# Kernel tuning notes

Hardware: AMD Instinct MI355X
Metric: run time of the kernel (lower is better)

Reference implementation:

```python
import jax, jax.numpy as jnp
import numpy as np

B, D, H = 8192, 1024, 1024


def _linear_init(key, shape, fan_in):
    bound = 1.0 / np.sqrt(fan_in)
    return jax.random.uniform(key, shape, jnp.float32, -bound, bound)


def setup_inputs() -> dict:
    key = jax.random.key(0)
    ks = jax.random.split(key, 20)
    inp = {
        "x": jax.random.normal(ks[0], (B, D), jnp.float32),
        "h_prev": jax.random.normal(ks[1], (B, H), jnp.float32),
        "c_prev": jax.random.normal(ks[2], (B, H), jnp.float32),
        "C_prev": jax.random.normal(ks[3], (B, H), jnp.float32),
        "n_prev": jax.random.uniform(ks[4], (B, H), jnp.float32),
        "m_prev": jax.random.normal(ks[5], (B, H), jnp.float32),
    }
    # input projections Wz/Wi/Wf/Wo: Linear(D -> H) with bias
    for i, g in enumerate("ziofo"[:4]):
        pass
    names = ["z", "i", "f", "o"]
    for j, g in enumerate(names):
        inp[f"W{g}"] = _linear_init(ks[6 + j], (H, D), D)
        inp[f"b{g}"] = _linear_init(ks[10 + j], (H,), D)
        inp[f"R{g}"] = _linear_init(ks[14 + j], (H, H), H)  # no bias
    return inp


def reference(x, h_prev, c_prev, C_prev, n_prev, m_prev,
              Wz, bz, Wi, bi, Wf, bf, Wo, bo,
              Rz, Ri, Rf, Ro):
    # Batch the 4 input projections and 4 recurrent projections into 2 GEMMs.
    Wcat = jnp.concatenate([Wi, Wf, Wo, Wz], axis=0)        # [4H, D]
    bcat = jnp.concatenate([bi, bf, bo, bz], axis=0)        # [4H]
    Rcat = jnp.concatenate([Ri, Rf, Ro, Rz], axis=0)        # [4H, H]
    pre = x @ Wcat.T + bcat + h_prev @ Rcat.T               # [B, 4H]
    pi, pf, po, pz = jnp.split(pre, 4, axis=1)

    i = jnp.exp(pi)
    f = jax.nn.sigmoid(pf)
    o = jax.nn.sigmoid(po)
    z = jnp.tanh(pz)

    c = f * c_prev + i * z
    n = f * n_prev + i
    m = jnp.maximum(jnp.log(f) + m_prev, pi)  # log(exp(pi)) == pi
    h = o * (c / n)
    return (h, c, C_prev, n, m)
```

## Files before the change

### kernel.cpp

```cpp
#include <hip/hip_runtime.h>


#define B_SZ 8192
#define D_SZ 1024
#define H_SZ 1024
#define K_SZ 2048
#define N4H  4096

typedef __attribute__((ext_vector_type(4))) float f32x4;
typedef _Float16 f16;
typedef __attribute__((ext_vector_type(8))) f16 f16x8;
typedef unsigned short u16;
typedef __attribute__((ext_vector_type(4))) unsigned short u16x4;

static __device__ __forceinline__ u16 f2h(float f) {
    f16 h = (f16)f;
    return __builtin_bit_cast(unsigned short, h);
}

static __device__ __forceinline__ float rcp_fast(float x) {
    float r;
    asm("v_rcp_f32 %0, %1" : "=v"(r) : "v"(x));
    return r;
}

static __device__ __forceinline__ void load_lds16(const void* g, void* l) {
    __builtin_amdgcn_global_load_lds(
        (const __attribute__((address_space(1))) void*)g,
        (__attribute__((address_space(3))) void*)l, 16, 0, 0);
}

__global__ void convert_AW(const float* __restrict__ x, const float* __restrict__ h,
                           const float* __restrict__ Wi, const float* __restrict__ Wf,
                           const float* __restrict__ Wo, const float* __restrict__ Wz,
                           const float* __restrict__ Ri, const float* __restrict__ Rf,
                           const float* __restrict__ Ro, const float* __restrict__ Rz,
                           const float* __restrict__ C_prev,
                           u16* __restrict__ A, u16* __restrict__ Wb,
                           float* __restrict__ outC) {
    const size_t nvecA = (size_t)B_SZ * K_SZ / 4;
    const size_t nvecW = (size_t)N4H * K_SZ / 4;
    const size_t nvecC = (size_t)B_SZ * H_SZ / 4;
    const size_t nvec  = nvecA + nvecW + nvecC;
    const size_t stride = (size_t)gridDim.x * blockDim.x;
    for (size_t v = (size_t)blockIdx.x * blockDim.x + threadIdx.x; v < nvec; v += stride) {
        if (v >= nvecA + nvecW) {
            size_t e = (v - nvecA - nvecW) * 4;
            *(f32x4*)&outC[e] = *(const f32x4*)&C_prev[e];
            continue;
        }
        const float* src;
        u16* dst;
        if (v < nvecA) {
            size_t e = v * 4;
            size_t row = e >> 11;
            int col = (int)(e & 2047);
            src = (col < D_SZ) ? (x + row * D_SZ + col)
                               : (h + row * H_SZ + (col - D_SZ));
            dst = A + e;
        } else {
            size_t e = (v - nvecA) * 4;
            size_t r = e >> 11;
            int col = (int)(e & 2047);
            int g = (int)(r >> 4) & 3;
            int j = (int)((r >> 6) << 4) | (int)(r & 15);
            const float* Wg = (g == 0) ? Wi : (g == 1) ? Wf : (g == 2) ? Wo : Wz;
            const float* Rg = (g == 0) ? Ri : (g == 1) ? Rf : (g == 2) ? Ro : Rz;
            src = (col < D_SZ) ? (Wg + (size_t)j * D_SZ + col)
                               : (Rg + (size_t)j * H_SZ + (col - D_SZ));
            dst = Wb + e;
        }
        f32x4 val = *(const f32x4*)src;
        u16x4 o;
        o[0] = f2h(val[0]); o[1] = f2h(val[1]); o[2] = f2h(val[2]); o[3] = f2h(val[3]);
        *(u16x4*)dst = o;
    }
}

__global__ __launch_bounds__(256, 2)
void gemm_fused(const u16* __restrict__ A, const u16* __restrict__ W,
                const float* __restrict__ c_prev, const float* __restrict__ n_prev,
                const float* __restrict__ m_prev,
                const float* __restrict__ bi, const float* __restrict__ bfv,
                const float* __restrict__ bo, const float* __restrict__ bz,
                float* __restrict__ out) {
    __shared__ char smem[49152];
    u16* lA = (u16*)smem;
    u16* lB = (u16*)(smem + 16384);
    float* eC = (float*)smem;
    float* eN = (float*)(smem + 16384);
    float* eM = (float*)(smem + 32768);

    const int tid = threadIdx.x;
    const int w  = tid >> 6;
    const int l  = tid & 63;
    const int wm = w >> 1;
    const int wn = w & 1;
    const int m0 = blockIdx.x * 128;
    const int n0 = blockIdx.y * 128;

    const int lrow8 = l >> 3;
    const int lseg  = (l & 7) ^ lrow8;

    const int fr = l & 15;
    const int kq = l >> 4;

    f32x4 acc[4][4] = {};

    for (int kt = 0; kt < K_SZ; kt += 64) {
#pragma unroll
        for (int r = 0; r < 4; ++r) {
            int rowA = r * 32 + w * 8 + lrow8;
            const u16* gA = A + (size_t)(m0 + rowA) * K_SZ + kt + lseg * 8;
            load_lds16(gA, (char*)lA + (r * 32 + w * 8) * 128);
            const u16* gB = W + (size_t)(n0 + rowA) * K_SZ + kt + lseg * 8;
            load_lds16(gB, (char*)lB + (r * 32 + w * 8) * 128);
        }
        __syncthreads();

#pragma unroll
        for (int ks = 0; ks < 2; ++ks) {
            f16x8 af[4], bfr[4];
#pragma unroll
            for (int mi = 0; mi < 4; ++mi) {
                int row = wm * 64 + mi * 16 + fr;
                int seg = (ks * 4 + kq) ^ (row & 7);
                af[mi] = *(const f16x8*)&lA[row * 64 + seg * 8];
            }
#pragma unroll
            for (int ni = 0; ni < 4; ++ni) {
                int row = wn * 64 + ni * 16 + fr;
                int seg = (ks * 4 + kq) ^ (row & 7);
                bfr[ni] = *(const f16x8*)&lB[row * 64 + seg * 8];
            }
#pragma unroll
            for (int mi = 0; mi < 4; ++mi)
#pragma unroll
                for (int ni = 0; ni < 4; ++ni)
                    acc[mi][ni] = __builtin_amdgcn_mfma_f32_16x16x32_f16(
                        af[mi], bfr[ni], acc[mi][ni], 0, 0, 0);
        }
        __syncthreads();
    }

    const int jbase = ((n0 + wn * 64) >> 6) * 16;
    {
        const size_t goff = (size_t)(m0 + wm * 64) * H_SZ + jbase;
        const float* cb = c_prev + goff;
        const float* nb = n_prev + goff;
        const float* mb = m_prev + goff;
        const size_t lsrc = (size_t)(l >> 2) * H_SZ + (l & 3) * 4;
#pragma unroll
        for (int k = 0; k < 4; ++k) {
            char* ldst_c = (char*)eC + w * 4096 + k * 1024;
            char* ldst_n = (char*)eN + w * 4096 + k * 1024;
            char* ldst_m = (char*)eM + w * 4096 + k * 1024;
            load_lds16(cb + (size_t)k * 16 * H_SZ + lsrc, ldst_c);
            load_lds16(nb + (size_t)k * 16 * H_SZ + lsrc, ldst_n);
            load_lds16(mb + (size_t)k * 16 * H_SZ + lsrc, ldst_m);
        }
    }

    const size_t BH = (size_t)B_SZ * H_SZ;
    const int j = jbase + fr;
    const float bvi = bi[j], bvf = bfv[j], bvo = bo[j], bvz = bz[j];

    asm volatile("s_waitcnt vmcnt(0)" ::: "memory");
    const int ebase = w * 1024;

#pragma unroll
    for (int mi = 0; mi < 4; ++mi) {
        const int rbase = m0 + wm * 64 + mi * 16 + kq * 4;
        const int erow0 = mi * 16 + kq * 4;
#pragma unroll
        for (int r2 = 0; r2 < 4; ++r2) {
            const size_t idx = (size_t)(rbase + r2) * H_SZ + j;
            const int eidx = ebase + (erow0 + r2) * 16 + fr;
            float pi = acc[mi][0][r2] + bvi;
            float pf = acc[mi][1][r2] + bvf;
            float po = acc[mi][2][r2] + bvo;
            float pz = acc[mi][3][r2] + bvz;
            float iv = __expf(pi);
            float fv = rcp_fast(1.0f + __expf(-pf));
            float ov = rcp_fast(1.0f + __expf(-po));
            float zv = 1.0f - 2.0f * rcp_fast(__expf(2.0f * pz) + 1.0f);
            float cv = fv * eC[eidx] + iv * zv;
            float nv = fv * eN[eidx] + iv;
            float mv = fmaxf(__logf(fv) + eM[eidx], pi);
            out[idx]          = ov * cv * rcp_fast(nv);
            out[BH + idx]     = cv;
            out[3 * BH + idx] = nv;
            out[4 * BH + idx] = mv;
        }
    }
}

extern "C" void kernel_launch(void* const* d_in, const int* in_sizes, int n_in,
                              void* d_out, int out_size, void* d_ws, size_t ws_size,
                              hipStream_t stream) {
    const float* x      = (const float*)d_in[0];
    const float* h_prev = (const float*)d_in[1];
    const float* c_prev = (const float*)d_in[2];
    const float* C_prev = (const float*)d_in[3];
    const float* n_prev = (const float*)d_in[4];
    const float* m_prev = (const float*)d_in[5];
    const float* Wz = (const float*)d_in[6];
    const float* bz = (const float*)d_in[7];
    const float* Rz = (const float*)d_in[8];
    const float* Wi = (const float*)d_in[9];
    const float* bi = (const float*)d_in[10];
    const float* Ri = (const float*)d_in[11];
    const float* Wf = (const float*)d_in[12];
    const float* bf = (const float*)d_in[13];
    const float* Rf = (const float*)d_in[14];
    const float* Wo = (const float*)d_in[15];
    const float* bo = (const float*)d_in[16];
    const float* Ro = (const float*)d_in[17];
    float* out = (float*)d_out;

    const size_t BH = (size_t)B_SZ * H_SZ;

    u16* Abuf = (u16*)d_ws;
    u16* Wbuf = (u16*)((char*)d_ws + (size_t)32 * 1024 * 1024);

    convert_AW<<<2048, 256, 0, stream>>>(x, h_prev, Wi, Wf, Wo, Wz,
                                         Ri, Rf, Ro, Rz, C_prev,
                                         Abuf, Wbuf, out + 2 * BH);

    gemm_fused<<<dim3(B_SZ / 128, N4H / 128), 256, 0, stream>>>(
        Abuf, Wbuf, c_prev, n_prev, m_prev, bi, bf, bo, bz, out);
}
```

Before: 210.4 us.

## Enlarge GEMM block tile to 256x128 with 512 threads and split epilogue

Doubles the M tile per block to 256 rows using 8 waves, so each block loads the W tile once for twice as many rows and global traffic for B drops. LDS is repartitioned into a 32KB A region and a 16KB B region. The epilogue now stages c/n/m_prev in two halves so the per-wave staging fits the reused LDS. Launch bounds of (512,4) put heavy pressure on the register budget and risk spills, while the grid halves in size, which could hurt load balance.

```diff
diff --git a/kernel.cpp b/kernel.cpp
--- a/kernel.cpp
+++ b/kernel.cpp
@@ -77,7 +77,7 @@
     }
 }
 
-__global__ __launch_bounds__(256, 2)
+__global__ __launch_bounds__(512, 4)
 void gemm_fused(const u16* __restrict__ A, const u16* __restrict__ W,
                 const float* __restrict__ c_prev, const float* __restrict__ n_prev,
                 const float* __restrict__ m_prev,
@@ -86,17 +86,14 @@
                 float* __restrict__ out) {
     __shared__ char smem[49152];
     u16* lA = (u16*)smem;
-    u16* lB = (u16*)(smem + 16384);
-    float* eC = (float*)smem;
-    float* eN = (float*)(smem + 16384);
-    float* eM = (float*)(smem + 32768);
+    u16* lB = (u16*)(smem + 32768);
 
     const int tid = threadIdx.x;
     const int w  = tid >> 6;
     const int l  = tid & 63;
     const int wm = w >> 1;
     const int wn = w & 1;
-    const int m0 = blockIdx.x * 128;
+    const int m0 = blockIdx.x * 256;
     const int n0 = blockIdx.y * 128;
 
     const int lrow8 = l >> 3;
@@ -107,17 +104,22 @@
 
     f32x4 acc[4][4] = {};
 
-    for (int kt = 0; kt < K_SZ; kt += 64) {
+    auto stage = [&](int kt) {
 #pragma unroll
         for (int r = 0; r < 4; ++r) {
-            int rowA = r * 32 + w * 8 + lrow8;
-            const u16* gA = A + (size_t)(m0 + rowA) * K_SZ + kt + lseg * 8;
-            load_lds16(gA, (char*)lA + (r * 32 + w * 8) * 128);
-            const u16* gB = W + (size_t)(n0 + rowA) * K_SZ + kt + lseg * 8;
-            load_lds16(gB, (char*)lB + (r * 32 + w * 8) * 128);
-        }
-        __syncthreads();
-
+            int row = r * 64 + w * 8 + lrow8;
+            const u16* gA = A + (size_t)(m0 + row) * K_SZ + kt + lseg * 8;
+            load_lds16(gA, (char*)lA + (r * 64 + w * 8) * 128);
+        }
+#pragma unroll
+        for (int r = 0; r < 2; ++r) {
+            int row = r * 64 + w * 8 + lrow8;
+            const u16* gB = W + (size_t)(n0 + row) * K_SZ + kt + lseg * 8;
+            load_lds16(gB, (char*)lB + (r * 64 + w * 8) * 128);
+        }
+    };
+
+    auto compute = [&]() {
 #pragma unroll
         for (int ks = 0; ks < 2; ++ks) {
             f16x8 af[4], bfr[4];
@@ -140,42 +142,47 @@
                     acc[mi][ni] = __builtin_amdgcn_mfma_f32_16x16x32_f16(
                         af[mi], bfr[ni], acc[mi][ni], 0, 0, 0);
         }
+    };
+
+    for (int kt = 0; kt < K_SZ; kt += 64) {
+        stage(kt);
+        __syncthreads();
+        compute();
         __syncthreads();
     }
 
     const int jbase = ((n0 + wn * 64) >> 6) * 16;
-    {
-        const size_t goff = (size_t)(m0 + wm * 64) * H_SZ + jbase;
-        const float* cb = c_prev + goff;
-        const float* nb = n_prev + goff;
-        const float* mb = m_prev + goff;
-        const size_t lsrc = (size_t)(l >> 2) * H_SZ + (l & 3) * 4;
-#pragma unroll
-        for (int k = 0; k < 4; ++k) {
-            char* ldst_c = (char*)eC + w * 4096 + k * 1024;
-            char* ldst_n = (char*)eN + w * 4096 + k * 1024;
-            char* ldst_m = (char*)eM + w * 4096 + k * 1024;
-            load_lds16(cb + (size_t)k * 16 * H_SZ + lsrc, ldst_c);
-            load_lds16(nb + (size_t)k * 16 * H_SZ + lsrc, ldst_n);
-            load_lds16(mb + (size_t)k * 16 * H_SZ + lsrc, ldst_m);
-        }
-    }
-
-    const size_t BH = (size_t)B_SZ * H_SZ;
+    const size_t lsrc = (size_t)(l >> 2) * H_SZ + (l & 3) * 4;
+    const size_t gbase = (size_t)(m0 + wm * 64) * H_SZ + jbase;
+
+    auto issueHalf = [&](int hh) {
+        const size_t s0 = gbase + (size_t)hh * 32 * H_SZ + lsrc;
+#pragma unroll
+        for (int k = 0; k < 2; ++k) {
+            const size_t s = s0 + (size_t)k * 16 * H_SZ;
+            load_lds16(c_prev + s, smem +     0 + w * 2048 + k * 1024);
+            load_lds16(n_prev + s, smem + 16384 + w * 2048 + k * 1024);
+            load_lds16(m_prev + s, smem + 32768 + w * 2048 + k * 1024);
+        }
+    };
+
+    issueHalf(0);
     const int j = jbase + fr;
     const float bvi = bi[j], bvf = bfv[j], bvo = bo[j], bvz = bz[j];
 
-    asm volatile("s_waitcnt vmcnt(0)" ::: "memory");
-    const int ebase = w * 1024;
-
-#pragma unroll
-    for (int mi = 0; mi < 4; ++mi) {
+    const size_t BH = (size_t)B_SZ * H_SZ;
+    const float* eC = (const float*)(smem);
+    const float* eN = (const float*)(smem + 16384);
+    const float* eM = (const float*)(smem + 32768);
+    const int ebase = w * 512;
+
+    auto epiRound = [&](int mi) {
+        const int mi2 = mi & 1;
         const int rbase = m0 + wm * 64 + mi * 16 + kq * 4;
-        const int erow0 = mi * 16 + kq * 4;
 #pragma unroll
         for (int r2 = 0; r2 < 4; ++r2) {
             const size_t idx = (size_t)(rbase + r2) * H_SZ + j;
-            const int eidx = ebase + (erow0 + r2) * 16 + fr;
+            const int eidx = ebase + (mi2 * 16 + kq * 4 + r2) * 16 + fr;
             float pi = acc[mi][0][r2] + bvi;
             float pf = acc[mi][1][r2] + bvf;
             float po = acc[mi][2][r2] + bvo;
@@ -192,7 +199,15 @@
             out[3 * BH + idx] = nv;
             out[4 * BH + idx] = mv;
         }
-    }
+    };
+
+    asm volatile("s_waitcnt vmcnt(0)" ::: "memory");
+    epiRound(0);
+    epiRound(1);
+    issueHalf(1);
+    asm volatile("s_waitcnt vmcnt(0)" ::: "memory");
+    epiRound(2);
+    epiRound(3);
 }
 
 extern "C" void kernel_launch(void* const* d_in, const int* in_sizes, int n_in,
@@ -227,6 +242,6 @@
                                          Ri, Rf, Ro, Rz, C_prev,
                                          Abuf, Wbuf, out + 2 * BH);
 
-    gemm_fused<<<dim3(B_SZ / 128, N4H / 128), 256, 0, stream>>>(
+    gemm_fused<<<dim3(B_SZ / 256, N4H / 128), 512, 0, stream>>>(
         Abuf, Wbuf, c_prev, n_prev, m_prev, bi, bf, bo, bz, out);
 }
```

After: 284.4 us. 1.35x slower.
